# Optimization experiments

Hardware: AMD Instinct MI355X
Metric: run time of the kernel (lower is better)

The kernel has to match this reference:

```python
import jax, jax.numpy as jnp
import numpy as np

H = 64  # rnn_size == input_size
CANVAS = 25


def _init_params(key, vocab_size):
    ks = jax.random.split(key, 14)
    s = 0.05
    p = {}
    p['embed'] = jax.random.normal(ks[0], (vocab_size + 1, H), jnp.float32) * s
    p['W_ih'] = jax.random.normal(ks[1], (4 * H, H), jnp.float32) * s
    p['W_hh'] = jax.random.normal(ks[2], (4 * H, H), jnp.float32) * s
    p['b_ih'] = jax.random.normal(ks[3], (4 * H,), jnp.float32) * s
    p['b_hh'] = jax.random.normal(ks[4], (4 * H,), jnp.float32) * s
    p['Wc'] = jax.random.normal(ks[5], (3, H), jnp.float32) * s
    p['bc'] = jax.random.normal(ks[6], (3,), jnp.float32) * s
    p['Ws'] = jax.random.normal(ks[7], (3, H), jnp.float32) * s
    p['bs'] = jax.random.normal(ks[8], (3,), jnp.float32) * s
    p['Wo'] = jax.random.normal(ks[9], (2, H), jnp.float32) * s
    p['bo'] = jax.random.normal(ks[10], (2,), jnp.float32) * s
    p['Wr1'] = jax.random.normal(ks[11], (32, H + 1 + 4), jnp.float32) * s
    p['br1'] = jnp.zeros((32,), jnp.float32)
    p['Wr2'] = jax.random.normal(ks[12], (1, 32), jnp.float32) * s
    p['br2'] = jnp.zeros((1,), jnp.float32)
    return p


def setup_inputs() -> dict:
    key = jax.random.key(0)
    k1, k2, k3, k4, k5 = jax.random.split(key, 5)
    B, T, V = 4096, 128, 32000
    inp = {
        'inst': jax.random.randint(k1, (B, T), 0, V, dtype=jnp.int64)
        if jax.config.jax_enable_x64 else jax.random.randint(k1, (B, T), 0, V, dtype=jnp.int32),
        'prev_canvas': jax.random.normal(k2, (B, CANVAS, 4), jnp.float32),
        'ref_obj': jax.random.normal(k3, (B, 4), jnp.float32),
        'target_obj': jax.random.normal(k4, (B, 4), jnp.float32),
    }
    inp.update(_init_params(k5, V))
    return inp


def _encode(inst, embed, W_ih, W_hh, b_ih, b_hh):
    # inst: [B, T] -> h: [B, H] via sequential LSTMCell
    xs = embed[inst]                       # [B, T, H]
    xs = jnp.swapaxes(xs, 0, 1)            # [T, B, H]
    B = inst.shape[0]
    h0 = jnp.zeros((B, H), xs.dtype)
    c0 = jnp.zeros((B, H), xs.dtype)

    def step(carry, x):
        h, c = carry
        gates = x @ W_ih.T + b_ih + h @ W_hh.T + b_hh   # [B, 4H]
        i, f, g, o = jnp.split(gates, 4, axis=-1)
        i, f, o = jax.nn.sigmoid(i), jax.nn.sigmoid(f), jax.nn.sigmoid(o)
        c = f * c + i * jnp.tanh(g)
        h = o * jnp.tanh(c)
        return (h, c), None

    (h, _), _ = jax.lax.scan(step, (h0, c0), xs)
    return h


def _act_tag(inst):
    # 1.0 if last token with value >= 1 equals 9, else 0.0
    T = inst.shape[1]
    mask = inst >= 1                                   # [B, T]
    last_pos = T - 1 - jnp.argmax(mask[:, ::-1], axis=1)
    last_val = jnp.take_along_axis(inst, last_pos[:, None], axis=1)[:, 0]
    tag = jnp.where((last_val == 9) & mask.any(axis=1), 1.0, 0.0)
    return tag.astype(jnp.float32)


def reference(inst, prev_canvas, ref_obj, target_obj, embed, W_ih, W_hh, b_ih, b_hh,
              Wc, bc, Ws, bs, Wo, bo, Wr1, br1, Wr2, br2):
    h = _encode(inst, embed, W_ih, W_hh, b_ih, b_hh)           # [B, H]
    tag = _act_tag(inst)                                       # [B]
    inst2 = jnp.concatenate([h, tag[:, None]], axis=1)         # [B, H+1]
    inst2 = jnp.broadcast_to(inst2[:, None, :], (h.shape[0], CANVAS, H + 1))
    feat = jnp.concatenate([inst2, prev_canvas], axis=2)       # [B, 25, 69]
    hid = jax.nn.relu(jnp.einsum('bnf,of->bno', feat, Wr1) + br1)
    score = (jnp.einsum('bno,ro->bnr', hid, Wr2) + br2)[..., 0]  # [B, 25]
    weight = jax.nn.softmax(score, axis=1)
    ref_pred = jnp.einsum('bn,bnd->bd', weight, prev_canvas)   # [B, 4]
    offset = jnp.clip(h @ Wo.T + bo, -1.0, 1.0)                # hardtanh, [B, 2]
    color_out = jax.nn.log_softmax(h @ Wc.T + bc, axis=1)      # [B, 3]
    shape_out = jax.nn.log_softmax(h @ Ws.T + bs, axis=1)      # [B, 3]
    row_out = ref_pred[:, 2] + offset[:, 0]
    col_out = ref_pred[:, 3] + offset[:, 1]
    return (color_out, shape_out, row_out, col_out)
```

## Files before the change

### kernel.cpp

```cpp
#include <hip/hip_runtime.h>
#include <hip/hip_bf16.h>

#define HH 64
#define TT 128
#define TP 132
#define BT 16

typedef __attribute__((ext_vector_type(8))) short bf16x8;
typedef __attribute__((ext_vector_type(4))) float f32x4;

__device__ __forceinline__ unsigned short f2bf(float f) {
  union { float f; unsigned u; } v; v.f = f;
  return (unsigned short)((v.u + 0x8000u) >> 16);
}
__device__ __forceinline__ float rcp_(float x) { return __builtin_amdgcn_rcpf(x); }
__device__ __forceinline__ float exp2_(float x) { return __builtin_amdgcn_exp2f(x); }

#define L2E 1.44269504f
#define L2E2 2.88539008f

__device__ __forceinline__ float red32(float v) {
#pragma unroll
  for (int s = 16; s; s >>= 1) v += __shfl_xor(v, s, 32);
  return v;
}

__global__ void convert_embed(const float* __restrict__ src,
                              unsigned short* __restrict__ dst, int n) {
  int base = (blockIdx.x * 256 + threadIdx.x) * 4;
  if (base + 4 <= n) {
    float4 v = *(const float4*)(src + base);
    ushort4 r;
    r.x = f2bf(v.x); r.y = f2bf(v.y); r.z = f2bf(v.z); r.w = f2bf(v.w);
    *(ushort4*)(dst + base) = r;
  } else {
    for (int k = base; k < n; k++) dst[k] = f2bf(src[k]);
  }
}

#define MFMA(acc, a, b) acc = __builtin_amdgcn_mfma_f32_16x16x32_bf16(a, b, acc, 0, 0, 0)

__global__ __launch_bounds__(256, 1) void lstm_k(
    const int* __restrict__ inst, const unsigned short* __restrict__ ebf,
    const float* __restrict__ Wih, const float* __restrict__ Whh,
    const float* __restrict__ bih, const float* __restrict__ bhh,
    const float* __restrict__ canvas,
    const float* __restrict__ Wc, const float* __restrict__ bc,
    const float* __restrict__ Ws, const float* __restrict__ bs,
    const float* __restrict__ Wo, const float* __restrict__ bo,
    const float* __restrict__ Wr1, const float* __restrict__ br1,
    const float* __restrict__ Wr2, const float* __restrict__ br2,
    float* __restrict__ out, int B)
{
  __shared__ int tokT[BT * TP];
  __shared__ unsigned short hsh[2 * BT * HH];
  __shared__ float h_s[BT][68];
  __shared__ float Wr1_s[32 * 69];
  __shared__ float cv_s[BT * 100];

  const int tid  = threadIdx.x;
  const int lane = tid & 63;
  const int w    = tid >> 6;
  const int fr   = lane & 15;
  const int fg   = lane >> 4;
  const int b0   = blockIdx.x * BT;
  const int jcol = w * 16 + fr;

  for (int i = tid; i < BT * TT; i += 256) {
    const int b = i >> 7, t = i & (TT - 1);
    tokT[b * TP + t] = inst[(size_t)(b0 + b) * TT + t];
  }
  for (int i = tid; i < BT * HH; i += 256) hsh[i] = 0;
  for (int i = tid; i < 32 * 69; i += 256) Wr1_s[i] = Wr1[i];
  for (int i = tid; i < BT * 100; i += 256) cv_s[i] = canvas[(size_t)b0 * 100 + i];

  bf16x8 wt[4][2][2];
#pragma unroll
  for (int q = 0; q < 4; q++) {
    const int n = (w + q * 4) * 16 + fr;
#pragma unroll
    for (int kt = 0; kt < 2; kt++) {
      const float* pa = Wih + n * 64 + kt * 32 + fg * 8;
      const float* pb = Whh + n * 64 + kt * 32 + fg * 8;
      bf16x8 fa, fb;
#pragma unroll
      for (int j = 0; j < 8; j++) {
        union { float f; unsigned u; } va, vb; va.f = pa[j]; vb.f = pb[j];
        fa[j] = (short)((va.u + 0x8000u) >> 16);
        fb[j] = (short)((vb.u + 0x8000u) >> 16);
      }
      wt[q][kt][0] = fa; wt[q][kt][1] = fb;
    }
  }
  const float nbi = -L2E  * (bih[jcol]       + bhh[jcol]);
  const float nbf = -L2E  * (bih[64 + jcol]  + bhh[64 + jcol]);
  const float sbg =  L2E2 * (bih[128 + jcol] + bhh[128 + jcol]);
  const float nbo = -L2E  * (bih[192 + jcol] + bhh[192 + jcol]);

  const int sx = (fr & 7) << 4;
  const int ra = (fr * 128 + fg * 16) ^ sx;
  const int rb = (fr * 128 + 64 + fg * 16) ^ sx;
  int wa[4];
#pragma unroll
  for (int r = 0; r < 4; r++) {
    const int m = fg * 4 + r;
    wa[r] = (m * 128 + 2 * jcol) ^ ((m & 7) << 4);
  }
  char* const hs0 = (char*)hsh;
  char* const hs1 = hs0 + BT * HH * 2;
  const int* const tokrow = tokT + fr * TP;

  __syncthreads();

  bf16x8 xa0, xa1;
  {
    const int tk = tokrow[0];
    const unsigned short* p = ebf + tk * 64 + fg * 8;
    xa0 = *(const bf16x8*)p; xa1 = *(const bf16x8*)(p + 32);
  }
  float cst[4] = {0.f, 0.f, 0.f, 0.f};
  float hk[4];
  const f32x4 z4 = {0.f, 0.f, 0.f, 0.f};

#define LSTM_STEP(RD, WR, T)                                                   \
  {                                                                            \
    const int tknext = tokrow[((T) + 1) & (TT - 1)];                           \
    bf16x8 ha0 = *(const bf16x8*)((RD) + ra);                                  \
    bf16x8 ha1 = *(const bf16x8*)((RD) + rb);                                  \
    f32x4 D0 = z4, D1 = z4, D2 = z4, D3 = z4;                                  \
    MFMA(D0, xa0, wt[0][0][0]); MFMA(D0, xa1, wt[0][1][0]);                    \
    MFMA(D1, xa0, wt[1][0][0]); MFMA(D1, xa1, wt[1][1][0]);                    \
    MFMA(D2, xa0, wt[2][0][0]); MFMA(D2, xa1, wt[2][1][0]);                    \
    MFMA(D3, xa0, wt[3][0][0]); MFMA(D3, xa1, wt[3][1][0]);                    \
    const unsigned short* px = ebf + tknext * 64 + fg * 8;                     \
    bf16x8 xn0 = *(const bf16x8*)px;                                           \
    bf16x8 xn1 = *(const bf16x8*)(px + 32);                                    \
    MFMA(D0, ha0, wt[0][0][1]); MFMA(D0, ha1, wt[0][1][1]);                    \
    MFMA(D1, ha0, wt[1][0][1]); MFMA(D1, ha1, wt[1][1][1]);                    \
    MFMA(D2, ha0, wt[2][0][1]); MFMA(D2, ha1, wt[2][1][1]);                    \
    MFMA(D3, ha0, wt[3][0][1]); MFMA(D3, ha1, wt[3][1][1]);                    \
    _Pragma("unroll")                                                          \
    for (int r = 0; r < 4; r++) {                                              \
      const float pi = exp2_(fmaf(D0[r], -L2E, nbi));               \
      const float pf = exp2_(fmaf(D1[r], -L2E, nbf));               \
      const float eg = exp2_(fmaf(D2[r], L2E2, sbg));               \
      const float po = exp2_(fmaf(D3[r], -L2E, nbo));               \
      const float a  = (eg - 1.f) * rcp_((1.f + pi) * (eg + 1.f));             \
      const float c  = fmaf(rcp_(1.f + pf), cst[r], a);                        \
      cst[r] = c;                                                              \
      const float ec = exp2_(fminf(L2E2 * c, 60.f));                \
      const float hn = (ec - 1.f) * rcp_((1.f + po) * (ec + 1.f));             \
      hk[r] = hn;                                                              \
      union { float f; unsigned u; } cv; cv.f = hn;                            \
      *(unsigned short*)((WR) + wa[r]) = (unsigned short)((cv.u + 0x8000u) >> 16); \
    }                                                                          \
    __syncthreads();                                                           \
    xa0 = xn0; xa1 = xn1;                                                      \
  }

  for (int t = 0; t < TT; t += 2) {
    LSTM_STEP(hs0, hs1, t);
    LSTM_STEP(hs1, hs0, t + 1);
  }
#undef LSTM_STEP

#pragma unroll
  for (int r = 0; r < 4; r++) h_s[fg * 4 + r][jcol] = hk[r];
  __syncthreads();

  for (int p = 0; p < 2; p++) {
    const int m  = p * 8 + (tid >> 5);
    const int o  = tid & 31;
    const int gb = b0 + m;

    int key = -1;
#pragma unroll
    for (int q = 0; q < 4; q++) {
      const int t = o + q * 32;
      const int tk = tokT[m * TP + t];
      if (tk >= 1) key = max(key, (t << 16) | tk);
    }
#pragma unroll
    for (int s = 16; s; s >>= 1) key = max(key, __shfl_xor(key, s, 32));
    const float tag = (key >= 0 && (key & 0xFFFF) == 9) ? 1.f : 0.f;

    float base = br1[o] + Wr1_s[o * 69 + 64] * tag;
    for (int f = 0; f < 64; f++) base += Wr1_s[o * 69 + f] * h_s[m][f];
    const float wr2o = Wr2[o];
    const float* cv = cv_s + m * 100;

    float sc[25];
    float mx = -1e30f;
#pragma unroll
    for (int n = 0; n < 25; n++) {
      float acc = base;
#pragma unroll
      for (int d = 0; d < 4; d++) acc += Wr1_s[o * 69 + 65 + d] * cv[n * 4 + d];
      float pp = wr2o * fmaxf(acc, 0.f);
#pragma unroll
      for (int s = 16; s; s >>= 1) pp += __shfl_xor(pp, s, 32);
      sc[n] = pp + br2[0];
      mx = fmaxf(mx, sc[n]);
    }
    float sum = 0.f, rp2 = 0.f, rp3 = 0.f;
#pragma unroll
    for (int n = 0; n < 25; n++) {
      const float e = __expf(sc[n] - mx);
      sum += e;
      rp2 += e * cv[n * 4 + 2];
      rp3 += e * cv[n * 4 + 3];
    }
    const float inv = 1.f / sum;

    const float h0 = h_s[m][o], h1 = h_s[m][o + 32];
    float c0 = red32(h0 * Wc[o]       + h1 * Wc[32 + o])  + bc[0];
    float c1 = red32(h0 * Wc[64 + o]  + h1 * Wc[96 + o])  + bc[1];
    float c2 = red32(h0 * Wc[128 + o] + h1 * Wc[160 + o]) + bc[2];
    float s0 = red32(h0 * Ws[o]       + h1 * Ws[32 + o])  + bs[0];
    float s1 = red32(h0 * Ws[64 + o]  + h1 * Ws[96 + o])  + bs[1];
    float s2 = red32(h0 * Ws[128 + o] + h1 * Ws[160 + o]) + bs[2];
    float o0 = red32(h0 * Wo[o]       + h1 * Wo[32 + o])  + bo[0];
    float o1 = red32(h0 * Wo[64 + o]  + h1 * Wo[96 + o])  + bo[1];
    o0 = fminf(fmaxf(o0, -1.f), 1.f);
    o1 = fminf(fmaxf(o1, -1.f), 1.f);

    const float cm = fmaxf(c0, fmaxf(c1, c2));
    const float cl = cm + __logf(__expf(c0 - cm) + __expf(c1 - cm) + __expf(c2 - cm));
    const float sm = fmaxf(s0, fmaxf(s1, s2));
    const float sl = sm + __logf(__expf(s0 - sm) + __expf(s1 - sm) + __expf(s2 - sm));

    if (o == 0) {
      out[gb * 3 + 0] = c0 - cl; out[gb * 3 + 1] = c1 - cl; out[gb * 3 + 2] = c2 - cl;
      float* shp = out + (size_t)3 * B;
      shp[gb * 3 + 0] = s0 - sl; shp[gb * 3 + 1] = s1 - sl; shp[gb * 3 + 2] = s2 - sl;
      out[(size_t)6 * B + gb] = rp2 * inv + o0;
      out[(size_t)7 * B + gb] = rp3 * inv + o1;
    }
  }
}

extern "C" void kernel_launch(void* const* d_in, const int* in_sizes, int n_in,
                              void* d_out, int out_size, void* d_ws, size_t ws_size,
                              hipStream_t stream) {
  const int*   inst   = (const int*)  d_in[0];
  const float* canvas = (const float*)d_in[1];
  const float* embed  = (const float*)d_in[4];
  const float* Wih    = (const float*)d_in[5];
  const float* Whh    = (const float*)d_in[6];
  const float* bih    = (const float*)d_in[7];
  const float* bhh    = (const float*)d_in[8];
  const float* Wc     = (const float*)d_in[9];
  const float* bc     = (const float*)d_in[10];
  const float* Ws_    = (const float*)d_in[11];
  const float* bs     = (const float*)d_in[12];
  const float* Wo     = (const float*)d_in[13];
  const float* bo     = (const float*)d_in[14];
  const float* Wr1    = (const float*)d_in[15];
  const float* br1    = (const float*)d_in[16];
  const float* Wr2    = (const float*)d_in[17];
  const float* br2    = (const float*)d_in[18];

  const int B  = in_sizes[0] / TT;
  const int NE = in_sizes[4];

  unsigned short* ebf = (unsigned short*)d_ws;

  convert_embed<<<(NE / 4 + 255) / 256, 256, 0, stream>>>(embed, ebf, NE);
  lstm_k<<<B / BT, 256, 0, stream>>>(inst, ebf, Wih, Whh, bih, bhh,
                                     canvas, Wc, bc, Ws_, bs, Wo, bo,
                                     Wr1, br1, Wr2, br2, (float*)d_out, B);
}
```

Before: 98.66 us.

## Precompute per-vocab input projection table and drop Wih MFMAs from recurrence

A new kernel computes embed@W_ih^T for the whole vocabulary into a bf16 table in gate-interleaved layout, replacing the plain bf16 conversion of the embedding table. The recurrent loop then only runs the W_hh MFMAs and adds gathered projection values, halving matrix work on the serial critical path. Gathers are prefetched two steps ahead, and __syncthreads is swapped for an lgkmcnt wait plus a raw barrier. The trade-off is a larger precompute (about 32k x 256 outputs, roughly 16MB written) and an extra bf16 rounding of the input projection.

```diff
diff --git a/kernel.cpp b/kernel.cpp
--- a/kernel.cpp
+++ b/kernel.cpp
@@ -5,6 +5,7 @@
 #define TT 128
 #define TP 132
 #define BT 16
+#define NVOC 32001
 
 typedef __attribute__((ext_vector_type(8))) short bf16x8;
 typedef __attribute__((ext_vector_type(4))) float f32x4;
@@ -13,6 +14,9 @@
   union { float f; unsigned u; } v; v.f = f;
   return (unsigned short)((v.u + 0x8000u) >> 16);
 }
+__device__ __forceinline__ float bfh(unsigned short u) {
+  union { float f; unsigned u; } v; v.u = ((unsigned)u) << 16; return v.f;
+}
 __device__ __forceinline__ float rcp_(float x) { return __builtin_amdgcn_rcpf(x); }
 __device__ __forceinline__ float exp2_(float x) { return __builtin_amdgcn_exp2f(x); }
 
@@ -25,24 +29,43 @@
   return v;
 }
 
-__global__ void convert_embed(const float* __restrict__ src,
-                              unsigned short* __restrict__ dst, int n) {
-  int base = (blockIdx.x * 256 + threadIdx.x) * 4;
-  if (base + 4 <= n) {
-    float4 v = *(const float4*)(src + base);
-    ushort4 r;
-    r.x = f2bf(v.x); r.y = f2bf(v.y); r.z = f2bf(v.z); r.w = f2bf(v.w);
-    *(ushort4*)(dst + base) = r;
-  } else {
-    for (int k = base; k < n; k++) dst[k] = f2bf(src[k]);
-  }
-}
-
 #define MFMA(acc, a, b) acc = __builtin_amdgcn_mfma_f32_16x16x32_bf16(a, b, acc, 0, 0, 0)
 
+__global__ __launch_bounds__(256) void xproj_k(
+    const float* __restrict__ embed, const float* __restrict__ Wih,
+    unsigned short* __restrict__ xp)
+{
+  const int tid = threadIdx.x, lane = tid & 63, w = tid >> 6;
+  const int fr = lane & 15, fg = lane >> 4;
+  const int mt = blockIdx.x * 4 + w;
+  if (mt >= 2001) return;
+  const int tb = mt * 16;
+  int ta = tb + fr; if (ta > NVOC - 1) ta = NVOC - 1;
+  const float* ea = embed + (size_t)ta * 64 + fg * 8;
+  bf16x8 a0, a1;
+#pragma unroll
+  for (int j = 0; j < 8; j++) { a0[j] = (short)f2bf(ea[j]); a1[j] = (short)f2bf(ea[32 + j]); }
+  const f32x4 z4 = {0.f, 0.f, 0.f, 0.f};
+  for (int nt = 0; nt < 16; nt++) {
+    const int n = nt * 16 + fr;
+    const int q = n & 3, jj = n >> 2;
+    const float* wp = Wih + (size_t)(q * 64 + jj) * 64 + fg * 8;
+    bf16x8 b0, b1;
+#pragma unroll
+    for (int j = 0; j < 8; j++) { b0[j] = (short)f2bf(wp[j]); b1[j] = (short)f2bf(wp[32 + j]); }
+    f32x4 D = z4;
+    MFMA(D, a0, b0); MFMA(D, a1, b1);
+#pragma unroll
+    for (int r = 0; r < 4; r++) {
+      const int tk = tb + fg * 4 + r;
+      if (tk < NVOC) xp[(size_t)tk * 256 + n] = f2bf(D[r]);
+    }
+  }
+}
+
 __global__ __launch_bounds__(256, 1) void lstm_k(
-    const int* __restrict__ inst, const unsigned short* __restrict__ ebf,
-    const float* __restrict__ Wih, const float* __restrict__ Whh,
+    const int* __restrict__ inst, const unsigned short* __restrict__ xp,
+    const float* __restrict__ Whh,
     const float* __restrict__ bih, const float* __restrict__ bhh,
     const float* __restrict__ canvas,
     const float* __restrict__ Wc, const float* __restrict__ bc,
@@ -74,22 +97,16 @@
   for (int i = tid; i < 32 * 69; i += 256) Wr1_s[i] = Wr1[i];
   for (int i = tid; i < BT * 100; i += 256) cv_s[i] = canvas[(size_t)b0 * 100 + i];
 
-  bf16x8 wt[4][2][2];
+  bf16x8 whh[4][2];
 #pragma unroll
   for (int q = 0; q < 4; q++) {
-    const int n = (w + q * 4) * 16 + fr;
 #pragma unroll
     for (int kt = 0; kt < 2; kt++) {
-      const float* pa = Wih + n * 64 + kt * 32 + fg * 8;
-      const float* pb = Whh + n * 64 + kt * 32 + fg * 8;
-      bf16x8 fa, fb;
-#pragma unroll
-      for (int j = 0; j < 8; j++) {
-        union { float f; unsigned u; } va, vb; va.f = pa[j]; vb.f = pb[j];
-        fa[j] = (short)((va.u + 0x8000u) >> 16);
-        fb[j] = (short)((vb.u + 0x8000u) >> 16);
-      }
-      wt[q][kt][0] = fa; wt[q][kt][1] = fb;
+      const float* pb = Whh + (size_t)(q * 64 + jcol) * 64 + kt * 32 + fg * 8;
+      bf16x8 fb;
+#pragma unroll
+      for (int j = 0; j < 8; j++) fb[j] = (short)f2bf(pb[j]);
+      whh[q][kt] = fb;
     }
   }
   const float nbi = -L2E  * (bih[jcol]       + bhh[jcol]);
@@ -100,67 +117,79 @@
   const int sx = (fr & 7) << 4;
   const int ra = (fr * 128 + fg * 16) ^ sx;
   const int rb = (fr * 128 + 64 + fg * 16) ^ sx;
-  int wa[4];
+  int wa[4], tokOff[4];
 #pragma unroll
   for (int r = 0; r < 4; r++) {
     const int m = fg * 4 + r;
     wa[r] = (m * 128 + 2 * jcol) ^ ((m & 7) << 4);
+    tokOff[r] = m * TP;
   }
   char* const hs0 = (char*)hsh;
   char* const hs1 = hs0 + BT * HH * 2;
-  const int* const tokrow = tokT + fr * TP;
+  const int jc4 = jcol << 2;
 
   __syncthreads();
 
-  bf16x8 xa0, xa1;
-  {
-    const int tk = tokrow[0];
-    const unsigned short* p = ebf + tk * 64 + fg * 8;
-    xa0 = *(const bf16x8*)p; xa1 = *(const bf16x8*)(p + 32);
-  }
+  ushort4 xpA[4], xpB[4];
+#pragma unroll
+  for (int r = 0; r < 4; r++)
+    xpA[r] = *(const ushort4*)(xp + (size_t)tokT[tokOff[r] + 0] * 256 + jc4);
+#pragma unroll
+  for (int r = 0; r < 4; r++)
+    xpB[r] = *(const ushort4*)(xp + (size_t)tokT[tokOff[r] + 1] * 256 + jc4);
+
   float cst[4] = {0.f, 0.f, 0.f, 0.f};
   float hk[4];
   const f32x4 z4 = {0.f, 0.f, 0.f, 0.f};
 
-#define LSTM_STEP(RD, WR, T)                                                   \
+#define LSTM_STEP(XPC, RD, WR, T)                                              \
   {                                                                            \
-    const int tknext = tokrow[((T) + 1) & (TT - 1)];                           \
     bf16x8 ha0 = *(const bf16x8*)((RD) + ra);                                  \
     bf16x8 ha1 = *(const bf16x8*)((RD) + rb);                                  \
+    const int tn = ((T) + 2 < TT) ? (T) + 2 : TT - 1;                          \
+    const int k0 = tokT[tokOff[0] + tn];                                       \
+    const int k1 = tokT[tokOff[1] + tn];                                       \
+    const int k2 = tokT[tokOff[2] + tn];                                       \
+    const int k3 = tokT[tokOff[3] + tn];                                       \
     f32x4 D0 = z4, D1 = z4, D2 = z4, D3 = z4;                                  \
-    MFMA(D0, xa0, wt[0][0][0]); MFMA(D0, xa1, wt[0][1][0]);                    \
-    MFMA(D1, xa0, wt[1][0][0]); MFMA(D1, xa1, wt[1][1][0]);                    \
-    MFMA(D2, xa0, wt[2][0][0]); MFMA(D2, xa1, wt[2][1][0]);                    \
-    MFMA(D3, xa0, wt[3][0][0]); MFMA(D3, xa1, wt[3][1][0]);                    \
-    const unsigned short* px = ebf + tknext * 64 + fg * 8;                     \
-    bf16x8 xn0 = *(const bf16x8*)px;                                           \
-    bf16x8 xn1 = *(const bf16x8*)(px + 32);                                    \
-    MFMA(D0, ha0, wt[0][0][1]); MFMA(D0, ha1, wt[0][1][1]);                    \
-    MFMA(D1, ha0, wt[1][0][1]); MFMA(D1, ha1, wt[1][1][1]);                    \
-    MFMA(D2, ha0, wt[2][0][1]); MFMA(D2, ha1, wt[2][1][1]);                    \
-    MFMA(D3, ha0, wt[3][0][1]); MFMA(D3, ha1, wt[3][1][1]);                    \
+    MFMA(D0, ha0, whh[0][0]); MFMA(D0, ha1, whh[0][1]);                        \
+    MFMA(D1, ha0, whh[1][0]); MFMA(D1, ha1, whh[1][1]);                        \
+    MFMA(D2, ha0, whh[2][0]); MFMA(D2, ha1, whh[2][1]);                        \
+    MFMA(D3, ha0, whh[3][0]); MFMA(D3, ha1, whh[3][1]);                        \
+    float aI[4], aF[4], aG[4], aO[4];                                          \
     _Pragma("unroll")                                                          \
     for (int r = 0; r < 4; r++) {                                              \
-      const float pi = exp2_(fmaf(D0[r], -L2E, nbi));               \
-      const float pf = exp2_(fmaf(D1[r], -L2E, nbf));               \
-      const float eg = exp2_(fmaf(D2[r], L2E2, sbg));               \
-      const float po = exp2_(fmaf(D3[r], -L2E, nbo));               \
+      aI[r] = D0[r] + bfh(XPC[r].x);                                           \
+      aF[r] = D1[r] + bfh(XPC[r].y);                                           \
+      aG[r] = D2[r] + bfh(XPC[r].z);                                           \
+      aO[r] = D3[r] + bfh(XPC[r].w);                                           \
+    }                                                                          \
+    XPC[0] = *(const ushort4*)(xp + (size_t)k0 * 256 + jc4);                   \
+    XPC[1] = *(const ushort4*)(xp + (size_t)k1 * 256 + jc4);                   \
+    XPC[2] = *(const ushort4*)(xp + (size_t)k2 * 256 + jc4);                   \
+    XPC[3] = *(const ushort4*)(xp + (size_t)k3 * 256 + jc4);                   \
+    _Pragma("unroll")                                                          \
+    for (int r = 0; r < 4; r++) {                                              \
+      const float pi = exp2_(fmaf(aI[r], -L2E, nbi));                          \
+      const float pf = exp2_(fmaf(aF[r], -L2E, nbf));                          \
+      const float eg = exp2_(fmaf(aG[r],  L2E2, sbg));                         \
+      const float po = exp2_(fmaf(aO[r], -L2E, nbo));                          \
       const float a  = (eg - 1.f) * rcp_((1.f + pi) * (eg + 1.f));             \
       const float c  = fmaf(rcp_(1.f + pf), cst[r], a);                        \
       cst[r] = c;                                                              \
-      const float ec = exp2_(fminf(L2E2 * c, 60.f));                \
+      const float ec = exp2_(fminf(L2E2 * c, 60.f));                           \
       const float hn = (ec - 1.f) * rcp_((1.f + po) * (ec + 1.f));             \
       hk[r] = hn;                                                              \
       union { float f; unsigned u; } cv; cv.f = hn;                            \
       *(unsigned short*)((WR) + wa[r]) = (unsigned short)((cv.u + 0x8000u) >> 16); \
     }                                                                          \
-    __syncthreads();                                                           \
-    xa0 = xn0; xa1 = xn1;                                                      \
+    asm volatile("s_waitcnt lgkmcnt(0)" ::: "memory");                         \
+    __builtin_amdgcn_s_barrier();                                              \
   }
 
   for (int t = 0; t < TT; t += 2) {
-    LSTM_STEP(hs0, hs1, t);
-    LSTM_STEP(hs1, hs0, t + 1);
+    LSTM_STEP(xpA, hs0, hs1, t);
+    LSTM_STEP(xpB, hs1, hs0, t + 1);
   }
 #undef LSTM_STEP
 
@@ -260,13 +289,12 @@
   const float* Wr2    = (const float*)d_in[17];
   const float* br2    = (const float*)d_in[18];
 
-  const int B  = in_sizes[0] / TT;
-  const int NE = in_sizes[4];
-
-  unsigned short* ebf = (unsigned short*)d_ws;
-
-  convert_embed<<<(NE / 4 + 255) / 256, 256, 0, stream>>>(embed, ebf, NE);
-  lstm_k<<<B / BT, 256, 0, stream>>>(inst, ebf, Wih, Whh, bih, bhh,
+  const int B = in_sizes[0] / TT;
+
+  unsigned short* xp = (unsigned short*)d_ws;
+
+  xproj_k<<<501, 256, 0, stream>>>(embed, Wih, xp);
+  lstm_k<<<B / BT, 256, 0, stream>>>(inst, xp, Whh, bih, bhh,
                                      canvas, Wc, bc, Ws_, bs, Wo, bo,
                                      Wr1, br1, Wr2, br2, (float*)d_out, B);
 }
```

Result: slower. 116.5 us (+18.1%).
